# Performance work log

Hardware: AMD Instinct MI355X
Metric: run time of the kernel (lower is better)

## Reference

```python
import jax, jax.numpy as jnp
from jax import lax
import numpy as np


def _conv(x, w, b, pad):
    y = lax.conv_general_dilated(x, w, (1, 1), [(pad, pad), (pad, pad)],
                                 dimension_numbers=('NCHW', 'OIHW', 'NCHW'))
    return y + b[None, :, None, None]


def _bn(x, g, b, eps=1e-5):
    # training-mode batchnorm (batch statistics, biased variance) like torch default
    m = jnp.mean(x, (0, 2, 3), keepdims=True)
    v = jnp.mean((x - m) ** 2, (0, 2, 3), keepdims=True)
    return g[None, :, None, None] * (x - m) * lax.rsqrt(v + eps) + b[None, :, None, None]


def _maxpool2(x):
    return lax.reduce_window(x, -jnp.inf, lax.max, (1, 1, 2, 2), (1, 1, 2, 2), 'VALID')


def _power_features(x):
    # vectorized version of the per-image FFT + radial-bin histogram mean
    B, _, H, W = x.shape
    cy, cx = H // 2, W // 2
    yy, xx = jnp.meshgrid(jnp.arange(H), jnp.arange(W), indexing='ij')
    r = jnp.sqrt((xx - cx).astype(jnp.float32) ** 2 + (yy - cy).astype(jnp.float32) ** 2)
    max_r = min(H, W) // 2
    NB = 32
    r_bins = jnp.linspace(0.0, float(max_r), NB + 1)
    # bin j covers [r_bins[j], r_bins[j+1]) exactly as the torch mask
    idx = jnp.searchsorted(r_bins, r.ravel(), side='right') - 1
    valid = (idx >= 0) & (idx < NB)
    seg = jnp.where(valid, idx, NB)  # dump out-of-range into bin NB
    counts = jax.ops.segment_sum(valid.astype(jnp.float32), seg, NB + 1)[:NB]
    ps = jnp.abs(jnp.fft.fft2(x[:, 0])) ** 2  # [B,H,W]
    psf = ps.reshape(B, -1) * valid.astype(ps.dtype)[None, :]
    sums = jax.vmap(lambda p: jax.ops.segment_sum(p, seg, NB + 1))(psf)[:, :NB]
    radial = jnp.where(counts > 0, sums / jnp.maximum(counts, 1.0), 0.0)
    return jnp.log(radial + 1e-10)  # [B,32]


def reference(x, cw1, cb1, g1, bb1, cw2, cb2, g2, bb2, cw3, cb3, g3, bb3,
              cw4, cb4, g4, bb4, pcw, pcb, pg, pbb,
              pw1, pb1, pw2, pb2, pw3, pb3,
              fw1, fb1, fw2, fb2, fw3, fb3, fw4, fb4):
    h = jax.nn.relu(_bn(_conv(x, cw1, cb1, 2), g1, bb1)); h = _maxpool2(h)
    h = jax.nn.relu(_bn(_conv(h, cw2, cb2, 2), g2, bb2)); h = _maxpool2(h)
    h = jax.nn.relu(_bn(_conv(h, cw3, cb3, 1), g3, bb3)); h = _maxpool2(h)
    h = jax.nn.relu(_bn(_conv(h, cw4, cb4, 1), g4, bb4))        # [B,256,32,32]
    p = jax.nn.relu(_bn(_conv(h, pcw, pcb, 1), pg, pbb))        # [B,128,32,32]
    # adaptive avg pool (4,4): exact 8x8 windows, stride 8
    p = lax.reduce_window(p, 0.0, lax.add, (1, 1, 8, 8), (1, 1, 8, 8), 'VALID') / 64.0
    flat = p.reshape(p.shape[0], -1)  # [B,2048]
    pf = _power_features(x)           # [B,32]
    pf = jax.nn.relu(pf @ pw1.T + pb1)
    pf = jax.nn.relu(pf @ pw2.T + pb2)
    pf = jax.nn.relu(pf @ pw3.T + pb3)  # [B,64]
    c = jnp.concatenate([flat, pf], axis=1)  # [B,2112]
    c = jax.nn.relu(c @ fw1.T + fb1)
    c = jax.nn.relu(c @ fw2.T + fb2)
    c = jax.nn.relu(c @ fw3.T + fb3)
    return c @ fw4.T + fb4  # [B,2]


def setup_inputs() -> dict:
    key = jax.random.key(0)
    ki = iter(jax.random.split(key, 40))

    def W(shape):
        fan_in = int(np.prod(shape[1:]))
        return jax.random.normal(next(ki), shape, jnp.float32) / np.sqrt(fan_in)

    d = {'x': jax.random.normal(next(ki), (16, 1, 256, 256), jnp.float32)}
    convs = [('cw1', 'cb1', 'g1', 'bb1', (32, 1, 5, 5)),
             ('cw2', 'cb2', 'g2', 'bb2', (64, 32, 5, 5)),
             ('cw3', 'cb3', 'g3', 'bb3', (128, 64, 3, 3)),
             ('cw4', 'cb4', 'g4', 'bb4', (256, 128, 3, 3)),
             ('pcw', 'pcb', 'pg', 'pbb', (128, 256, 3, 3))]
    for wn, bn, gn, ben, s in convs:
        d[wn] = W(s); d[bn] = jnp.zeros(s[0], jnp.float32)
        d[gn] = jnp.ones(s[0], jnp.float32); d[ben] = jnp.zeros(s[0], jnp.float32)
    lins = [('pw1', 'pb1', (256, 32)), ('pw2', 'pb2', (128, 256)), ('pw3', 'pb3', (64, 128)),
            ('fw1', 'fb1', (512, 2112)), ('fw2', 'fb2', (256, 512)),
            ('fw3', 'fb3', (128, 256)), ('fw4', 'fb4', (2, 128))]
    for wn, bn, s in lins:
        d[wn] = W(s); d[bn] = jnp.zeros(s[0], jnp.float32)
    return d
```

## Files before the change

### kernel.cpp

```cpp
#include <hip/hip_runtime.h>
#include <math.h>


#define PI2F 6.283185307179586f

typedef _Float16 half8 __attribute__((ext_vector_type(8)));
typedef _Float16 half4v __attribute__((ext_vector_type(4)));
typedef float f32x4 __attribute__((ext_vector_type(4)));


__device__ __forceinline__ int bitrev8(int x) {
  x = ((x & 0x0F) << 4) | ((x >> 4) & 0x0F);
  x = ((x & 0x33) << 2) | ((x >> 2) & 0x33);
  x = ((x & 0x55) << 1) | ((x >> 1) & 0x55);
  return x;
}

__global__ __launch_bounds__(64)
void fft_rows(const float* __restrict__ x, float2* __restrict__ out) {
  __shared__ float2 s[256];
  __shared__ float2 tw[128];
  int blk = blockIdx.x;
  const float* rowp = x + (size_t)blk * 256;
  int t = threadIdx.x;
  for (int i = t; i < 128; i += 64) {
    float sn, cs;
    sincosf(-(PI2F / 256.f) * (float)i, &sn, &cs);
    tw[i] = make_float2(cs, sn);
  }
  #pragma unroll
  for (int e = 0; e < 4; ++e) {
    int i = t + (e << 6);
    s[bitrev8(i)] = make_float2(rowp[i], 0.f);
  }
  __syncthreads();
  #pragma unroll
  for (int st = 1; st <= 8; ++st) {
    int half = 1 << (st - 1);
    #pragma unroll
    for (int j = 0; j < 2; ++j) {
      int bf = t + (j << 6);
      int pos = bf & (half - 1);
      int grp = bf >> (st - 1);
      int i0 = (grp << st) | pos;
      int i1 = i0 + half;
      int k = pos << (8 - st);
      float cs = tw[k].x, sn = tw[k].y;
      float2 a = s[i0], b = s[i1];
      float tr = cs * b.x - sn * b.y;
      float ti = cs * b.y + sn * b.x;
      s[i0] = make_float2(a.x + tr, a.y + ti);
      s[i1] = make_float2(a.x - tr, a.y - ti);
    }
    __syncthreads();
  }
  float2* op = out + (size_t)blk * 256;
  #pragma unroll
  for (int e = 0; e < 4; ++e) { int i = t + (e << 6); op[i] = s[i]; }
}

__device__ __forceinline__ int radial_bin(int r2) {
  int j = (int)(sqrtf((float)r2) * 0.25f);
  while ((j + 1) * (j + 1) * 16 <= r2) ++j;
  while (j > 0 && j * j * 16 > r2) --j;
  return j;
}

__global__ __launch_bounds__(256)
void fft_cols_radial_v2(const float2* __restrict__ f, float* __restrict__ radial) {
  __shared__ float2 s[8][258];
  __shared__ float2 tw[128];
  __shared__ float bins[8][32];
  int b = blockIdx.x >> 5;
  int col0 = (blockIdx.x & 31) * 8;
  int t = threadIdx.x;
  for (int i = t; i < 128; i += 256) {
    float sn, cs;
    sincosf(-(PI2F / 256.f) * (float)i, &sn, &cs);
    tw[i] = make_float2(cs, sn);
  }
  ((float*)bins)[t] = 0.f;
  for (int idx = t; idx < 2048; idx += 256) {
    int row = idx >> 3, c = idx & 7;
    s[c][bitrev8(row)] = f[(size_t)b * 65536 + row * 256 + col0 + c];
  }
  __syncthreads();
  int c = t >> 5, l = t & 31;
  float2* sc = &s[c][0];
  #pragma unroll
  for (int st = 1; st <= 8; ++st) {
    int half = 1 << (st - 1);
    #pragma unroll
    for (int j = 0; j < 4; ++j) {
      int bf = l + (j << 5);
      int pos = bf & (half - 1);
      int grp = bf >> (st - 1);
      int i0 = (grp << st) | pos;
      int i1 = i0 + half;
      int k = pos << (8 - st);
      float cs = tw[k].x, sn = tw[k].y;
      float2 a = sc[i0], bb = sc[i1];
      float tr = cs * bb.x - sn * bb.y;
      float ti = cs * bb.y + sn * bb.x;
      sc[i0] = make_float2(a.x + tr, a.y + ti);
      sc[i1] = make_float2(a.x - tr, a.y - ti);
    }
    __syncthreads();
  }
  int dx = col0 + c - 128;
  #pragma unroll
  for (int e = 0; e < 8; ++e) {
    int i = l * 8 + e;
    float2 v = sc[i];
    float ps = v.x * v.x + v.y * v.y;
    int dy = i - 128;
    int r2 = dx * dx + dy * dy;
    if (r2 < 16384) atomicAdd(&bins[c][radial_bin(r2)], ps);
  }
  __syncthreads();
  if (t < 32) {
    float s0 = bins[0][t] + bins[1][t] + bins[2][t] + bins[3][t] +
               bins[4][t] + bins[5][t] + bins[6][t] + bins[7][t];
    atomicAdd(&radial[b * 32 + t], s0);
  }
}

__device__ __forceinline__ int isqrt_(int v) {
  int r = (int)sqrtf((float)v);
  while (r * r > v) --r;
  while ((r + 1) * (r + 1) <= v) ++r;
  return r;
}

__global__ __launch_bounds__(256)
void radial_finalize_v3(const float* __restrict__ radial, float* __restrict__ pf0) {
  __shared__ int red[4];
  __shared__ int cnt_s;
  int j = blockIdx.x, t = threadIdx.x;
  int dy = t - 128;
  int lo = 16 * j * j, hi = 16 * (j + 1) * (j + 1);
  int d2 = dy * dy;
  int cnt = 0;
  int tHi = hi - 1 - d2;
  if (tHi >= 0) {
    int rHi = isqrt_(tHi);
    int nHi = min(rHi, 127) + min(rHi, 128) + 1;
    int nLo = 0;
    int tLo = lo - 1 - d2;
    if (tLo >= 0) { int rLo = isqrt_(tLo); nLo = min(rLo, 127) + min(rLo, 128) + 1; }
    cnt = nHi - nLo;
  }
  #pragma unroll
  for (int off = 32; off > 0; off >>= 1) cnt += __shfl_down(cnt, off);
  if ((t & 63) == 0) red[t >> 6] = cnt;
  __syncthreads();
  if (t == 0) cnt_s = red[0] + red[1] + red[2] + red[3];
  __syncthreads();
  if (t < 16) {
    float cf = (float)cnt_s;
    float sum = radial[t * 32 + j];
    float val = cf > 0.f ? sum / fmaxf(cf, 1.f) : 0.f;
    pf0[t * 32 + j] = logf(val + 1e-10f);
  }
}


__global__ __launch_bounds__(256)
void wtrans_all(const float* __restrict__ cw2, const float* __restrict__ cw3,
                const float* __restrict__ cw4, const float* __restrict__ pcw,
                _Float16* __restrict__ wb2, _Float16* __restrict__ wb3,
                _Float16* __restrict__ wb4, _Float16* __restrict__ wbp) {
  int blk = blockIdx.x;
  const float* src; _Float16* dst; int COUT, CIN, KK, i;
  if (blk < 200)       { src = cw2; dst = wb2; COUT = 64;  CIN = 32;  KK = 25; i = blk * 256; }
  else if (blk < 488)  { src = cw3; dst = wb3; COUT = 128; CIN = 64;  KK = 9;  i = (blk - 200) * 256; }
  else if (blk < 1640) { src = cw4; dst = wb4; COUT = 256; CIN = 128; KK = 9;  i = (blk - 488) * 256; }
  else                 { src = pcw; dst = wbp; COUT = 128; CIN = 256; KK = 9;  i = (blk - 1640) * 256; }
  i += threadIdx.x;
  if (i >= COUT * CIN * KK) return;
  int ci = i % CIN;
  int r = i / CIN;
  int co = r % COUT;
  int tap = r / COUT;
  dst[i] = (_Float16)src[((size_t)co * CIN + ci) * KK + tap];
}


__device__ __forceinline__ void load16(float* d, const float* p) {
  f32x4 v0 = *(const f32x4*)(p);
  f32x4 v1 = *(const f32x4*)(p + 4);
  f32x4 v2 = *(const f32x4*)(p + 8);
  f32x4 v3 = *(const f32x4*)(p + 12);
  #pragma unroll
  for (int e = 0; e < 4; ++e) { d[e] = v0[e]; d[4+e] = v1[e]; d[8+e] = v2[e]; d[12+e] = v3[e]; }
}

__global__ __launch_bounds__(256)
void conv1_fused(const float* __restrict__ x, const float* __restrict__ w,
                 _Float16* __restrict__ praw, size_t minoff,
                 float* __restrict__ stats) {
  __shared__ float lds[12 * 264];
  __shared__ float r1[4][32], r2[4][32];
  int t = threadIdx.x;
  int y0 = blockIdx.x * 8, n = blockIdx.y;
  const float* xp = x + (size_t)n * 65536;
  for (int i = t; i < 12 * 264; i += 256) {
    int r = i / 264, cc = i % 264;
    int gy = y0 + r - 2, gx = cc - 4;
    lds[i] = (gy >= 0 && gy < 256 && gx >= 0 && gx < 256) ? xp[gy * 256 + gx] : 0.f;
  }
  __syncthreads();
  int c = t & 31, xg = t >> 5;
  float wreg[25];
  #pragma unroll
  for (int k = 0; k < 25; ++k) wreg[k] = w[c * 25 + k];
  float s1 = 0.f, s2 = 0.f;
  for (int strip = 0; strip < 4; ++strip) {
    int px0 = xg * 8 + strip * 64;
    float f[5][16];
    #pragma unroll
    for (int rr = 0; rr < 4; ++rr) load16(f[rr], &lds[rr * 264 + px0]);
    float pmax[4], pmin[4];
    #pragma unroll
    for (int r = 0; r < 8; ++r) {
      load16(f[(r + 4) % 5], &lds[(r + 4) * 264 + px0]);
      f32x4 A = {0.f, 0.f, 0.f, 0.f}, B = {0.f, 0.f, 0.f, 0.f};
      #pragma unroll
      for (int ky = 0; ky < 5; ++ky) {
        const float* fr = f[(r + ky) % 5];
        #pragma unroll
        for (int kx = 0; kx < 5; ++kx) {
          float wv = wreg[ky * 5 + kx];
          f32x4 ia = {fr[2 + kx], fr[3 + kx], fr[4 + kx], fr[5 + kx]};
          f32x4 ib = {fr[6 + kx], fr[7 + kx], fr[8 + kx], fr[9 + kx]};
          A += wv * ia; B += wv * ib;
        }
      }
      s1 += A[0] + A[1] + A[2] + A[3] + B[0] + B[1] + B[2] + B[3];
      s2 += A[0]*A[0] + A[1]*A[1] + A[2]*A[2] + A[3]*A[3]
          + B[0]*B[0] + B[1]*B[1] + B[2]*B[2] + B[3]*B[3];
      float cm[4], cn[4];
      cm[0] = fmaxf(A[0], A[1]); cn[0] = fminf(A[0], A[1]);
      cm[1] = fmaxf(A[2], A[3]); cn[1] = fminf(A[2], A[3]);
      cm[2] = fmaxf(B[0], B[1]); cn[2] = fminf(B[0], B[1]);
      cm[3] = fmaxf(B[2], B[3]); cn[3] = fminf(B[2], B[3]);
      if ((r & 1) == 0) {
        #pragma unroll
        for (int k = 0; k < 4; ++k) { pmax[k] = cm[k]; pmin[k] = cn[k]; }
      } else {
        int prow = (y0 + r) >> 1;
        int pc0 = px0 >> 1;
        #pragma unroll
        for (int k = 0; k < 4; ++k) {
          size_t idx = (((size_t)n * 128 + prow) * 128 + pc0 + k) * 32 + c;
          praw[idx] = (_Float16)fmaxf(pmax[k], cm[k]);
          praw[minoff + idx] = (_Float16)fminf(pmin[k], cn[k]);
        }
      }
    }
  }
  s1 += __shfl_down(s1, 32);
  s2 += __shfl_down(s2, 32);
  if ((t & 63) < 32) { r1[t >> 6][t & 31] = s1; r2[t >> 6][t & 31] = s2; }
  __syncthreads();
  if (t < 32) {
    float* st = stats + (blockIdx.x & 7) * 64;
    atomicAdd(&st[t],      r1[0][t] + r1[1][t] + r1[2][t] + r1[3][t]);
    atomicAdd(&st[32 + t], r2[0][t] + r2[1][t] + r2[2][t] + r2[3][t]);
  }
}


template <int CIN, int COUT, int H, int W, int K, int TH, int TW, int CW,
          int COT, int PT, int SLAB, int INPOOL, int OUTPOOL>
__global__ __launch_bounds__(256)
void conv_mfma4(const _Float16* __restrict__ in, size_t in_minoff,
                const _Float16* __restrict__ wb,
                _Float16* __restrict__ out, size_t out_minoff,
                const float* __restrict__ instats, const float* __restrict__ ing,
                const float* __restrict__ inbb, float in_invN,
                float* __restrict__ stats) {
  constexpr int P = K / 2, R = TH + 2 * P, XW = TW + 2 * P, PIX = R * XW;
  constexpr int TAPS = K * K, CSP = SLAB + 8;
  constexpr int NCC = SLAB / 32, NPH = CIN / SLAB, SUBS = SLAB / 8;
  constexpr int PW = 4 / CW, COB = CW * 16 * COT;
  static_assert(TH * TW == PW * 16 * PT, "pos tile mismatch");
  static_assert(TW == 16, "row-per-fragment requires TW=16");
  static_assert(!OUTPOOL || (PT % 2 == 0), "pool needs even PT");
  __shared__ _Float16 lds[PIX * CSP];
  __shared__ float inscs[CIN], inshs[CIN];
  __shared__ float sst[2][COB];
  int t = threadIdx.x;
  int lane = t & 63, wv = t >> 6;
  int lane15 = lane & 15, quad = lane >> 4;
  constexpr int WT = W / TW;
  int x0 = (blockIdx.x % WT) * TW, y0 = (blockIdx.x / WT) * TH;
  int coB = blockIdx.y * COB;
  int nb = blockIdx.z;
  int co_off = (wv % CW) * (16 * COT);
  int rowbase = (wv / CW) * PT;

  for (int i = t; i < 2 * COB; i += 256) ((float*)sst)[i] = 0.f;
  for (int c = t; c < CIN; c += 256) {
    float s1 = 0.f, s2 = 0.f;
    #pragma unroll
    for (int s = 0; s < 8; ++s) {
      s1 += instats[s * 2 * CIN + c];
      s2 += instats[s * 2 * CIN + CIN + c];
    }
    float mean = s1 * in_invN;
    float var  = s2 * in_invN - mean * mean;
    float k = ing[c] / sqrtf(var + 1e-5f);
    inscs[c] = k; inshs[c] = inbb[c] - mean * k;
  }
  __syncthreads();

  f32x4 acc[COT][PT];
  #pragma unroll
  for (int ct = 0; ct < COT; ++ct)
    #pragma unroll
    for (int pt = 0; pt < PT; ++pt)
      #pragma unroll
      for (int e = 0; e < 4; ++e) acc[ct][pt][e] = 0.f;

  int bbase[PT];
  #pragma unroll
  for (int pt = 0; pt < PT; ++pt)
    bbase[pt] = ((rowbase + pt) * XW + lane15) * CSP + quad * 8;
  const _Float16* aptr[COT];
  #pragma unroll
  for (int ct = 0; ct < COT; ++ct)
    aptr[ct] = wb + (size_t)(coB + co_off + ct * 16 + lane15) * CIN + quad * 8;

  const size_t ibase = (size_t)nb * H * W * CIN;

  #pragma unroll
  for (int ph = 0; ph < NPH; ++ph) {
    constexpr int ITEMS = PIX * SUBS;
    for (int i = t; i < ITEMS; i += 256) {
      int sub = i % SUBS, pix = i / SUBS;
      int r = pix / XW, xx = pix % XW;
      int gy = y0 + r - P, gx = x0 + xx - P;
      int ch = ph * SLAB + sub * 8;
      half8 v;
      #pragma unroll
      for (int j = 0; j < 8; ++j) v[j] = (_Float16)0.f;
      if (gy >= 0 && gy < H && gx >= 0 && gx < W) {
        size_t off = ibase + ((size_t)gy * W + gx) * CIN + ch;
        half8 vmx = *(const half8*)(in + off);
        if (INPOOL) {
          half8 vmn = *(const half8*)(in + in_minoff + off);
          #pragma unroll
          for (int j = 0; j < 8; ++j) {
            float sc = inscs[ch + j];
            float xv = sc >= 0.f ? (float)vmx[j] : (float)vmn[j];
            v[j] = (_Float16)fmaxf(sc * xv + inshs[ch + j], 0.f);
          }
        } else {
          #pragma unroll
          for (int j = 0; j < 8; ++j) {
            float sc = inscs[ch + j];
            v[j] = (_Float16)fmaxf(sc * (float)vmx[j] + inshs[ch + j], 0.f);
          }
        }
      }
      *(half8*)(&lds[pix * CSP + sub * 8]) = v;
    }
    __syncthreads();
    #pragma unroll
    for (int cc = 0; cc < NCC; ++cc) {
      #pragma unroll
      for (int tap = 0; tap < TAPS; ++tap) {
        int ky = tap / K, kx = tap % K;
        half8 a[COT], b[PT];
        #pragma unroll
        for (int ct = 0; ct < COT; ++ct)
          a[ct] = *(const half8*)(aptr[ct] + (size_t)tap * COUT * CIN +
                                  ph * SLAB + cc * 32);
        #pragma unroll
        for (int pt = 0; pt < PT; ++pt)
          b[pt] = *(const half8*)(&lds[bbase[pt] + (ky * XW + kx) * CSP + cc * 32]);
        #pragma unroll
        for (int ct = 0; ct < COT; ++ct)
          #pragma unroll
          for (int pt = 0; pt < PT; ++pt)
            acc[ct][pt] = __builtin_amdgcn_mfma_f32_16x16x32_f16(
                a[ct], b[pt], acc[ct][pt], 0, 0, 0);
      }
    }
    if (ph + 1 < NPH) __syncthreads();
  }

  if (OUTPOOL) {
    #pragma unroll
    for (int ct = 0; ct < COT; ++ct)
      #pragma unroll
      for (int pp = 0; pp < PT; pp += 2) {
        half4v hmax, hmin;
        #pragma unroll
        for (int e = 0; e < 4; ++e) {
          float vmx = fmaxf(acc[ct][pp][e], acc[ct][pp + 1][e]);
          float vmn = fminf(acc[ct][pp][e], acc[ct][pp + 1][e]);
          float omx = fmaxf(vmx, __shfl_xor(vmx, 1));
          float omn = fminf(vmn, __shfl_xor(vmn, 1));
          hmax[e] = (_Float16)omx; hmin[e] = (_Float16)omn;
        }
        if ((lane15 & 1) == 0) {
          int co = coB + co_off + ct * 16 + quad * 4;
          int prow = (y0 + rowbase + pp) >> 1;
          int pcol = (x0 >> 1) + (lane15 >> 1);
          size_t idx = (((size_t)nb * (H / 2) + prow) * (W / 2) + pcol) * COUT + co;
          *(half4v*)(out + idx) = hmax;
          *(half4v*)(out + out_minoff + idx) = hmin;
        }
      }
  } else {
    #pragma unroll
    for (int ct = 0; ct < COT; ++ct)
      #pragma unroll
      for (int pt = 0; pt < PT; ++pt) {
        int co = coB + co_off + ct * 16 + quad * 4;
        int y = y0 + rowbase + pt, x = x0 + lane15;
        _Float16* op = out + (((size_t)nb * H + y) * W + x) * COUT + co;
        half4v h;
        #pragma unroll
        for (int e = 0; e < 4; ++e) h[e] = (_Float16)acc[ct][pt][e];
        *(half4v*)op = h;
      }
  }

  #pragma unroll
  for (int ct = 0; ct < COT; ++ct)
    #pragma unroll
    for (int e = 0; e < 4; ++e) {
      float sv = 0.f, sq = 0.f;
      #pragma unroll
      for (int pt = 0; pt < PT; ++pt) {
        float v = acc[ct][pt][e];
        sv += v; sq += v * v;
      }
      sv += __shfl_xor(sv, 1); sq += __shfl_xor(sq, 1);
      sv += __shfl_xor(sv, 2); sq += __shfl_xor(sq, 2);
      sv += __shfl_xor(sv, 4); sq += __shfl_xor(sq, 4);
      sv += __shfl_xor(sv, 8); sq += __shfl_xor(sq, 8);
      if (lane15 == 0) {
        int cl = co_off + ct * 16 + quad * 4 + e;
        atomicAdd(&sst[0][cl], sv);
        atomicAdd(&sst[1][cl], sq);
      }
    }
  __syncthreads();
  float* st = stats + (blockIdx.x & 7) * 2 * COUT;
  for (int i = t; i < COB; i += 256) {
    atomicAdd(&st[coB + i], sst[0][i]);
    atomicAdd(&st[COUT + coB + i], sst[1][i]);
  }
}


__global__ __launch_bounds__(256)
void bn_avgpool_concat(const _Float16* __restrict__ x, const float* __restrict__ stats,
                       const float* __restrict__ g, const float* __restrict__ bb,
                       float* __restrict__ concat, float invN) {
  __shared__ float scs[128], shs[128];
  int t = threadIdx.x;
  int n = blockIdx.y;
  for (int c = t; c < 128; c += 256) {
    float s1 = 0.f, s2 = 0.f;
    #pragma unroll
    for (int s = 0; s < 8; ++s) {
      s1 += stats[s * 256 + c];
      s2 += stats[s * 256 + 128 + c];
    }
    float mean = s1 * invN;
    float var  = s2 * invN - mean * mean;
    float k = g[c] / sqrtf(var + 1e-5f);
    scs[c] = k; shs[c] = bb[c] - mean * k;
  }
  __syncthreads();
  int i = blockIdx.x * 256 + t;
  int c = i & 127, opix = i >> 7;
  int py = opix >> 2, px = opix & 3;
  float sc = scs[c], sh = shs[c];
  float s = 0.f;
  for (int yy = 0; yy < 8; ++yy)
    #pragma unroll
    for (int xx = 0; xx < 8; ++xx)
      s += fmaxf((float)x[(((size_t)n * 32 + py * 8 + yy) * 32 + px * 8 + xx) * 128 + c] * sc + sh, 0.f);
  concat[(size_t)n * 2112 + c * 16 + opix] = s * (1.f / 64.f);
}


__global__ __launch_bounds__(64)
void linear_k(const float* __restrict__ in, const float* __restrict__ w,
              const float* __restrict__ bias, float* __restrict__ out,
              int I, int in_stride, int out_stride, int relu) {
  int o = blockIdx.x, b = blockIdx.y;
  int lane = threadIdx.x;
  const float* ip = in + (size_t)b * in_stride;
  const float* wp = w + (size_t)o * I;
  float acc = 0.f;
  for (int i = lane; i < I; i += 64) acc += ip[i] * wp[i];
  #pragma unroll
  for (int off = 32; off > 0; off >>= 1) acc += __shfl_down(acc, off);
  if (lane == 0) {
    float v = acc + bias[o];
    if (relu) v = fmaxf(v, 0.f);
    out[(size_t)b * out_stride + o] = v;
  }
}

__global__ __launch_bounds__(256)
void pf_mlp(const float* __restrict__ pf0,
            const float* __restrict__ pw1, const float* __restrict__ pb1,
            const float* __restrict__ pw2, const float* __restrict__ pb2,
            const float* __restrict__ pw3, const float* __restrict__ pb3,
            float* __restrict__ concat) {
  __shared__ float a0[32], a1[256], a2[128];
  int b = blockIdx.x, t = threadIdx.x;
  if (t < 32) a0[t] = pf0[b * 32 + t];
  __syncthreads();
  {
    float s = pb1[t];
    for (int i = 0; i < 32; ++i) s += pw1[t * 32 + i] * a0[i];
    a1[t] = fmaxf(s, 0.f);
  }
  __syncthreads();
  if (t < 128) {
    float s = pb2[t];
    for (int i = 0; i < 256; ++i) s += pw2[t * 256 + i] * a1[i];
    a2[t] = fmaxf(s, 0.f);
  }
  __syncthreads();
  if (t < 64) {
    float s = pb3[t];
    for (int i = 0; i < 128; ++i) s += pw3[t * 128 + i] * a2[i];
    concat[(size_t)b * 2112 + 2048 + t] = fmaxf(s, 0.f);
  }
}

__global__ __launch_bounds__(256)
void fc_tail(const float* __restrict__ fc1o,
             const float* __restrict__ fw2, const float* __restrict__ fb2,
             const float* __restrict__ fw3, const float* __restrict__ fb3,
             const float* __restrict__ fw4, const float* __restrict__ fb4,
             float* __restrict__ out) {
  __shared__ float a1[512], a2[256], a3[128];
  int b = blockIdx.x, t = threadIdx.x;
  a1[t] = fc1o[b * 512 + t];
  a1[t + 256] = fc1o[b * 512 + t + 256];
  __syncthreads();
  {
    float s = fb2[t];
    for (int i = 0; i < 512; ++i) s += fw2[t * 512 + i] * a1[i];
    a2[t] = fmaxf(s, 0.f);
  }
  __syncthreads();
  if (t < 128) {
    float s = fb3[t];
    for (int i = 0; i < 256; ++i) s += fw3[t * 256 + i] * a2[i];
    a3[t] = fmaxf(s, 0.f);
  }
  __syncthreads();
  if (t < 2) {
    float s = fb4[t];
    for (int i = 0; i < 128; ++i) s += fw4[t * 128 + i] * a3[i];
    out[b * 2 + t] = s;
  }
}


extern "C" void kernel_launch(void* const* d_in, const int* in_sizes, int n_in,
                              void* d_out, int out_size, void* d_ws, size_t ws_size,
                              hipStream_t stream) {
  (void)in_sizes; (void)n_in; (void)out_size; (void)ws_size;
  const float* x   = (const float*)d_in[0];
  const float* cw1 = (const float*)d_in[1];
  const float* g1  = (const float*)d_in[3];
  const float* bb1 = (const float*)d_in[4];
  const float* cw2 = (const float*)d_in[5];
  const float* g2  = (const float*)d_in[7];
  const float* bb2 = (const float*)d_in[8];
  const float* cw3 = (const float*)d_in[9];
  const float* g3  = (const float*)d_in[11];
  const float* bb3 = (const float*)d_in[12];
  const float* cw4 = (const float*)d_in[13];
  const float* g4  = (const float*)d_in[15];
  const float* bb4 = (const float*)d_in[16];
  const float* pcw = (const float*)d_in[17];
  const float* pg  = (const float*)d_in[19];
  const float* pbb = (const float*)d_in[20];
  const float* pw1 = (const float*)d_in[21];
  const float* pb1 = (const float*)d_in[22];
  const float* pw2 = (const float*)d_in[23];
  const float* pb2 = (const float*)d_in[24];
  const float* pw3 = (const float*)d_in[25];
  const float* pb3 = (const float*)d_in[26];
  const float* fw1 = (const float*)d_in[27];
  const float* fb1 = (const float*)d_in[28];
  const float* fw2 = (const float*)d_in[29];
  const float* fb2 = (const float*)d_in[30];
  const float* fw3 = (const float*)d_in[31];
  const float* fb3 = (const float*)d_in[32];
  const float* fw4 = (const float*)d_in[33];
  const float* fb4 = (const float*)d_in[34];

  char* base = (char*)d_ws;
  _Float16* pool1raw = (_Float16*)(base + 0);
  _Float16* pool3raw = (_Float16*)(base + 0);
  _Float16* pconvo   = (_Float16*)(base + 8388608);
  _Float16* pool2raw = (_Float16*)(base + 33554432);
  float2*   fftbuf   = (float2*)(base + 33554432);
  _Float16* conv4raw = (_Float16*)(base + 33554432);
  _Float16* wb2      = (_Float16*)(base + 50331648);
  _Float16* wb3      = (_Float16*)(base + 50434048);
  _Float16* wb4      = (_Float16*)(base + 50581504);
  _Float16* wbp      = (_Float16*)(base + 51171328);
  float*    zbase    = (float*)(base + 51761152);
  float*    stats1   = zbase;
  float*    stats2   = zbase + 512;
  float*    stats3   = zbase + 1536;
  float*    stats4   = zbase + 3584;
  float*    stats5   = zbase + 7680;
  float*    radial   = zbase + 9728;
  float*    pf0      = (float*)(base + 51802112);
  float*    concat   = (float*)(base + 51804160);
  float*    fc1o     = (float*)(base + 51939328);

  hipMemsetAsync(zbase, 0, 10240 * sizeof(float), stream);

  wtrans_all<<<2792, 256, 0, stream>>>(cw2, cw3, cw4, pcw, wb2, wb3, wb4, wbp);

  fft_rows<<<4096, 64, 0, stream>>>(x, fftbuf);
  fft_cols_radial_v2<<<512, 256, 0, stream>>>(fftbuf, radial);
  radial_finalize_v3<<<32, 256, 0, stream>>>(radial, pf0);
  pf_mlp<<<16, 256, 0, stream>>>(pf0, pw1, pb1, pw2, pb2, pw3, pb3, concat);

  conv1_fused<<<dim3(32, 16), 256, 0, stream>>>(x, cw1, pool1raw, 8388608, stats1);

  conv_mfma4<32, 64, 128, 128, 5, 8, 16, 2, 2, 4, 32, 1, 1>
      <<<dim3(128, 1, 16), 256, 0, stream>>>(
      pool1raw, 8388608, wb2, pool2raw, 4194304,
      stats1, g1, bb1, 1.f / 1048576.f, stats2);

  conv_mfma4<64, 128, 64, 64, 3, 8, 16, 2, 4, 4, 64, 1, 1>
      <<<dim3(32, 1, 16), 256, 0, stream>>>(
      pool2raw, 4194304, wb3, pool3raw, 2097152,
      stats2, g2, bb2, 1.f / 262144.f, stats3);

  conv_mfma4<128, 256, 32, 32, 3, 4, 16, 2, 2, 2, 128, 1, 0>
      <<<dim3(16, 4, 16), 256, 0, stream>>>(
      pool3raw, 2097152, wb4, conv4raw, 0,
      stats3, g3, bb3, 1.f / 65536.f, stats4);

  conv_mfma4<256, 128, 32, 32, 3, 4, 16, 2, 2, 2, 128, 0, 0>
      <<<dim3(16, 2, 16), 256, 0, stream>>>(
      conv4raw, 0, wbp, pconvo, 0,
      stats4, g4, bb4, 1.f / 16384.f, stats5);
  bn_avgpool_concat<<<dim3(8, 16), 256, 0, stream>>>(
      pconvo, stats5, pg, pbb, concat, 1.f / 16384.f);

  linear_k<<<dim3(512, 16), 64, 0, stream>>>(concat, fw1, fb1, fc1o, 2112, 2112, 512, 1);
  fc_tail<<<16, 256, 0, stream>>>(fc1o, fw2, fb2, fw3, fb3, fw4, fb4, (float*)d_out);
}
```

Baseline: 408.5 us.

## Split BN+ReLU application for layers 1-2 into standalone passes

Adds a bn_apply kernel that turns the pooled max/min fp16 outputs of conv1 and conv2 into normalized, ReLU'd activations once. Conv2 and conv3 then read the applied tensors directly, so they no longer redo the per-channel scale/shift on every halo-overlapping tile load and no longer read the min buffer. Conv1 tiles shrink from 8 to 4 rows to double block count, and the workspace layout is reshuffled to fit the extra buffers. The cost is an extra read/write pass over the pool1 and pool2 activations plus two more kernel launches.

```diff
diff --git a/kernel.cpp b/kernel.cpp
--- a/kernel.cpp
+++ b/kernel.cpp
@@ -199,12 +199,12 @@
 void conv1_fused(const float* __restrict__ x, const float* __restrict__ w,
                  _Float16* __restrict__ praw, size_t minoff,
                  float* __restrict__ stats) {
-  __shared__ float lds[12 * 264];
+  __shared__ float lds[8 * 264];
   __shared__ float r1[4][32], r2[4][32];
   int t = threadIdx.x;
-  int y0 = blockIdx.x * 8, n = blockIdx.y;
+  int y0 = blockIdx.x * 4, n = blockIdx.y;
   const float* xp = x + (size_t)n * 65536;
-  for (int i = t; i < 12 * 264; i += 256) {
+  for (int i = t; i < 8 * 264; i += 256) {
     int r = i / 264, cc = i % 264;
     int gy = y0 + r - 2, gx = cc - 4;
     lds[i] = (gy >= 0 && gy < 256 && gx >= 0 && gx < 256) ? xp[gy * 256 + gx] : 0.f;
@@ -222,7 +222,7 @@
     for (int rr = 0; rr < 4; ++rr) load16(f[rr], &lds[rr * 264 + px0]);
     float pmax[4], pmin[4];
     #pragma unroll
-    for (int r = 0; r < 8; ++r) {
+    for (int r = 0; r < 4; ++r) {
       load16(f[(r + 4) % 5], &lds[(r + 4) * 264 + px0]);
       f32x4 A = {0.f, 0.f, 0.f, 0.f}, B = {0.f, 0.f, 0.f, 0.f};
       #pragma unroll
@@ -271,10 +271,49 @@
 }
 
 
+__global__ __launch_bounds__(256)
+void bn_apply(const _Float16* __restrict__ raw, size_t minoff,
+              const float* __restrict__ stats, const float* __restrict__ g,
+              const float* __restrict__ bb, _Float16* __restrict__ out,
+              int C, int HWC, float invN) {
+  __shared__ float scs[64], shs[64];
+  int t = threadIdx.x, n = blockIdx.y;
+  for (int c = t; c < C; c += 256) {
+    float s1 = 0.f, s2 = 0.f;
+    #pragma unroll
+    for (int s = 0; s < 8; ++s) {
+      s1 += stats[s * 2 * C + c];
+      s2 += stats[s * 2 * C + C + c];
+    }
+    float mean = s1 * invN;
+    float var  = s2 * invN - mean * mean;
+    float k = g[c] / sqrtf(var + 1e-5f);
+    scs[c] = k; shs[c] = bb[c] - mean * k;
+  }
+  __syncthreads();
+  size_t basei = (size_t)n * HWC;
+  int nv = HWC >> 3;
+  for (int i = blockIdx.x * 256 + t; i < nv; i += gridDim.x * 256) {
+    size_t off = basei + ((size_t)i << 3);
+    half8 vmx = *(const half8*)(raw + off);
+    half8 vmn = *(const half8*)(raw + minoff + off);
+    int ch = (i << 3) & (C - 1);
+    half8 o;
+    #pragma unroll
+    for (int j = 0; j < 8; ++j) {
+      float sc = scs[ch + j];
+      float xv = sc >= 0.f ? (float)vmx[j] : (float)vmn[j];
+      o[j] = (_Float16)fmaxf(sc * xv + shs[ch + j], 0.f);
+    }
+    *(half8*)(out + off) = o;
+  }
+}
+
+
 template <int CIN, int COUT, int H, int W, int K, int TH, int TW, int CW,
-          int COT, int PT, int SLAB, int INPOOL, int OUTPOOL>
-__global__ __launch_bounds__(256)
-void conv_mfma4(const _Float16* __restrict__ in, size_t in_minoff,
+          int COT, int PT, int SLAB, int APPLY, int INPOOL, int OUTPOOL>
+__global__ __launch_bounds__(256)
+void conv_mfma5(const _Float16* __restrict__ in, size_t in_minoff,
                 const _Float16* __restrict__ wb,
                 _Float16* __restrict__ out, size_t out_minoff,
                 const float* __restrict__ instats, const float* __restrict__ ing,
@@ -288,7 +327,7 @@
   static_assert(TW == 16, "row-per-fragment requires TW=16");
   static_assert(!OUTPOOL || (PT % 2 == 0), "pool needs even PT");
   __shared__ _Float16 lds[PIX * CSP];
-  __shared__ float inscs[CIN], inshs[CIN];
+  __shared__ float inscs[APPLY ? CIN : 8], inshs[APPLY ? CIN : 8];
   __shared__ float sst[2][COB];
   int t = threadIdx.x;
   int lane = t & 63, wv = t >> 6;
@@ -301,19 +340,21 @@
   int rowbase = (wv / CW) * PT;
 
   for (int i = t; i < 2 * COB; i += 256) ((float*)sst)[i] = 0.f;
-  for (int c = t; c < CIN; c += 256) {
-    float s1 = 0.f, s2 = 0.f;
-    #pragma unroll
-    for (int s = 0; s < 8; ++s) {
-      s1 += instats[s * 2 * CIN + c];
-      s2 += instats[s * 2 * CIN + CIN + c];
-    }
-    float mean = s1 * in_invN;
-    float var  = s2 * in_invN - mean * mean;
-    float k = ing[c] / sqrtf(var + 1e-5f);
-    inscs[c] = k; inshs[c] = inbb[c] - mean * k;
-  }
-  __syncthreads();
+  if (APPLY) {
+    for (int c = t; c < CIN; c += 256) {
+      float s1 = 0.f, s2 = 0.f;
+      #pragma unroll
+      for (int s = 0; s < 8; ++s) {
+        s1 += instats[s * 2 * CIN + c];
+        s2 += instats[s * 2 * CIN + CIN + c];
+      }
+      float mean = s1 * in_invN;
+      float var  = s2 * in_invN - mean * mean;
+      float k = ing[c] / sqrtf(var + 1e-5f);
+      inscs[c] = k; inshs[c] = inbb[c] - mean * k;
+    }
+    __syncthreads();
+  }
 
   f32x4 acc[COT][PT];
   #pragma unroll
@@ -348,7 +389,9 @@
       if (gy >= 0 && gy < H && gx >= 0 && gx < W) {
         size_t off = ibase + ((size_t)gy * W + gx) * CIN + ch;
         half8 vmx = *(const half8*)(in + off);
-        if (INPOOL) {
+        if (!APPLY) {
+          v = vmx;
+        } else if (INPOOL) {
           half8 vmn = *(const half8*)(in + in_minoff + off);
           #pragma unroll
           for (int j = 0; j < 8; ++j) {
@@ -606,12 +649,14 @@
   const float* fb4 = (const float*)d_in[34];
 
   char* base = (char*)d_ws;
+  float2*   fftbuf   = (float2*)(base + 0);
   _Float16* pool1raw = (_Float16*)(base + 0);
+  _Float16* pool1app = (_Float16*)(base + 33554432);
+  _Float16* pool2raw = (_Float16*)(base + 0);
+  _Float16* pool2app = (_Float16*)(base + 16777216);
   _Float16* pool3raw = (_Float16*)(base + 0);
-  _Float16* pconvo   = (_Float16*)(base + 8388608);
-  _Float16* pool2raw = (_Float16*)(base + 33554432);
-  float2*   fftbuf   = (float2*)(base + 33554432);
-  _Float16* conv4raw = (_Float16*)(base + 33554432);
+  _Float16* conv4raw = (_Float16*)(base + 8388608);
+  _Float16* pconvo   = (_Float16*)(base + 16777216);
   _Float16* wb2      = (_Float16*)(base + 50331648);
   _Float16* wb3      = (_Float16*)(base + 50434048);
   _Float16* wb4      = (_Float16*)(base + 50581504);
@@ -636,24 +681,28 @@
   radial_finalize_v3<<<32, 256, 0, stream>>>(radial, pf0);
   pf_mlp<<<16, 256, 0, stream>>>(pf0, pw1, pb1, pw2, pb2, pw3, pb3, concat);
 
-  conv1_fused<<<dim3(32, 16), 256, 0, stream>>>(x, cw1, pool1raw, 8388608, stats1);
-
-  conv_mfma4<32, 64, 128, 128, 5, 8, 16, 2, 2, 4, 32, 1, 1>
+  conv1_fused<<<dim3(64, 16), 256, 0, stream>>>(x, cw1, pool1raw, 8388608, stats1);
+  bn_apply<<<dim3(128, 16), 256, 0, stream>>>(
+      pool1raw, 8388608, stats1, g1, bb1, pool1app, 32, 524288, 1.f / 1048576.f);
+
+  conv_mfma5<32, 64, 128, 128, 5, 8, 16, 2, 2, 4, 32, 0, 0, 1>
       <<<dim3(128, 1, 16), 256, 0, stream>>>(
-      pool1raw, 8388608, wb2, pool2raw, 4194304,
-      stats1, g1, bb1, 1.f / 1048576.f, stats2);
-
-  conv_mfma4<64, 128, 64, 64, 3, 8, 16, 2, 4, 4, 64, 1, 1>
+      pool1app, 0, wb2, pool2raw, 4194304,
+      nullptr, nullptr, nullptr, 0.f, stats2);
+  bn_apply<<<dim3(128, 16), 256, 0, stream>>>(
+      pool2raw, 4194304, stats2, g2, bb2, pool2app, 64, 262144, 1.f / 262144.f);
+
+  conv_mfma5<64, 128, 64, 64, 3, 8, 16, 2, 4, 4, 64, 0, 0, 1>
       <<<dim3(32, 1, 16), 256, 0, stream>>>(
-      pool2raw, 4194304, wb3, pool3raw, 2097152,
-      stats2, g2, bb2, 1.f / 262144.f, stats3);
-
-  conv_mfma4<128, 256, 32, 32, 3, 4, 16, 2, 2, 2, 128, 1, 0>
+      pool2app, 0, wb3, pool3raw, 2097152,
+      nullptr, nullptr, nullptr, 0.f, stats3);
+
+  conv_mfma5<128, 256, 32, 32, 3, 4, 16, 2, 2, 2, 128, 1, 1, 0>
       <<<dim3(16, 4, 16), 256, 0, stream>>>(
       pool3raw, 2097152, wb4, conv4raw, 0,
       stats3, g3, bb3, 1.f / 65536.f, stats4);
 
-  conv_mfma4<256, 128, 32, 32, 3, 4, 16, 2, 2, 2, 128, 0, 0>
+  conv_mfma5<256, 128, 32, 32, 3, 4, 16, 2, 2, 2, 128, 1, 0, 0>
       <<<dim3(16, 2, 16), 256, 0, stream>>>(
       conv4raw, 0, wbp, pconvo, 0,
       stats4, g4, bb4, 1.f / 16384.f, stats5);
```

Result: no change. 409.6 us (+0.3%).
